# Performance work log

Hardware: AMD Instinct MI355X
Metric: run time of the kernel (lower is better)

The kernel has to match this reference:

```python
import jax, jax.numpy as jnp
import numpy as np

D_MODEL = 768
NUM_HEADS = 12
HEAD_DIM = D_MODEL // NUM_HEADS
LN_EPS = 1e-5
MASK_NEG = -1000000.0


def setup_inputs() -> dict:
    key = jax.random.key(0)
    ks = jax.random.split(key, 10)
    B, L, S = 2, 2048, 2048
    s = 1.0 / np.sqrt(D_MODEL)
    return {
        "q": jax.random.normal(ks[0], (B, L, D_MODEL), jnp.float32),
        "k": jax.random.normal(ks[1], (B, S, D_MODEL), jnp.float32),
        "v": jax.random.normal(ks[2], (B, S, D_MODEL), jnp.float32),
        "attention_mask": jnp.ones((B, S), jnp.int32),
        "Wq": jax.random.normal(ks[3], (D_MODEL, D_MODEL), jnp.float32) * s,
        "Wk": jax.random.normal(ks[4], (D_MODEL, D_MODEL), jnp.float32) * s,
        "Wv": jax.random.normal(ks[5], (D_MODEL, D_MODEL), jnp.float32) * s,
        "W": jax.random.normal(ks[6], (D_MODEL, D_MODEL), jnp.float32) * s,
        "b": jnp.zeros((D_MODEL,), jnp.float32),
        "gamma": jnp.ones((D_MODEL,), jnp.float32),
        "beta": jnp.zeros((D_MODEL,), jnp.float32),
    }


def reference(q, k, v, attention_mask, Wq, Wk, Wv, W, b, gamma, beta):
    B, L, D = q.shape
    S = k.shape[1]
    H, hd = NUM_HEADS, HEAD_DIM
    # projections (torch Linear: x @ W^T), split heads -> (B,H,L,hd)
    Q = (q @ Wq.T).reshape(B, L, H, hd).transpose(0, 2, 1, 3)
    K = (k @ Wk.T).reshape(B, S, H, hd).transpose(0, 2, 1, 3)
    V = (v @ Wv.T).reshape(B, S, H, hd).transpose(0, 2, 1, 3)
    # scores (B,H,L,S) with additive key-padding mask
    scores = jnp.einsum("bhld,bhsd->bhls", Q, K) / np.sqrt(hd)
    mask_score = (1.0 - attention_mask.astype(q.dtype))[:, None, None, :] * MASK_NEG
    att = jax.nn.softmax(scores + mask_score, axis=-1)  # dropout p=0 (eval)
    # attend, merge heads, output projection (with bias)
    O = jnp.einsum("bhls,bhsd->bhld", att, V).transpose(0, 2, 1, 3).reshape(B, L, D)
    O = O @ W.T + b  # state dropout p=0 (eval)
    # residual + LayerNorm
    x = q + O
    mu = jnp.mean(x, axis=-1, keepdims=True)
    var = jnp.mean(jnp.square(x - mu), axis=-1, keepdims=True)
    return (x - mu) * jax.lax.rsqrt(var + LN_EPS) * gamma + beta
```

## Files before the change

### kernel.cpp

```cpp
#include <hip/hip_runtime.h>
#include <hip/hip_bf16.h>
#include <math.h>


typedef unsigned short u16;
typedef unsigned int   u32;
typedef __bf16 bf16x8 __attribute__((ext_vector_type(8)));
typedef float  f32x4  __attribute__((ext_vector_type(4)));

#define DM   768
#define MR   4096
#define WSZ  589824

#define LOG2E 1.44269504089f
#define SM_C  15.0f
#define K1    (0.125f * LOG2E)

__device__ inline u16 bfbits(float f) {
    union { __bf16 b; u16 u; } x; x.b = (__bf16)f; return x.u;
}

__device__ inline uint4 cvt8(const float* src) {
    const float4* p = reinterpret_cast<const float4*>(src);
    float4 a = p[0], b = p[1];
    union { __bf16 h[8]; uint4 v; } u;
    u.h[0] = (__bf16)a.x; u.h[1] = (__bf16)a.y; u.h[2] = (__bf16)a.z; u.h[3] = (__bf16)a.w;
    u.h[4] = (__bf16)b.x; u.h[5] = (__bf16)b.y; u.h[6] = (__bf16)b.z; u.h[7] = (__bf16)b.w;
    return u.v;
}

__device__ inline uint4 cvt8v(float4 a, float4 b) {
    union { __bf16 h[8]; uint4 v; } u;
    u.h[0] = (__bf16)a.x; u.h[1] = (__bf16)a.y; u.h[2] = (__bf16)a.z; u.h[3] = (__bf16)a.w;
    u.h[4] = (__bf16)b.x; u.h[5] = (__bf16)b.y; u.h[6] = (__bf16)b.z; u.h[7] = (__bf16)b.w;
    return u.v;
}

__global__ __launch_bounds__(256) void wcvt(
    const float* __restrict__ w0, const float* __restrict__ w1,
    const float* __restrict__ w2, const float* __restrict__ w3,
    u16* __restrict__ dst)
{
    const float* src = (blockIdx.y == 0) ? w0 : (blockIdx.y == 1) ? w1
                     : (blockIdx.y == 2) ? w2 : w3;
    size_t idx = ((size_t)blockIdx.x * 256 + threadIdx.x) * 8;
    *reinterpret_cast<uint4*>(&dst[(size_t)blockIdx.y * WSZ + idx]) = cvt8(&src[idx]);
}

__global__ __launch_bounds__(256, 2) void gemm_qkv(
    const float* __restrict__ xq, const float* __restrict__ xk, const float* __restrict__ xv,
    const u16* __restrict__ Wb4,
    u16* __restrict__ oq, u16* __restrict__ ok, u16* __restrict__ ov)
{
    const int mode = blockIdx.z;
    const float* X = (mode == 0) ? xq : (mode == 1) ? xk : xv;
    const u16* Wb  = Wb4 + (size_t)mode * WSZ;
    u16* out       = (mode == 0) ? oq : (mode == 1) ? ok : ov;

    __shared__ __attribute__((aligned(16))) u16 As[2][64][72];
    __shared__ __attribute__((aligned(16))) u16 Bs[2][64][72];

    const int tid  = threadIdx.x;
    const int lane = tid & 63;
    const int w    = tid >> 6;
    const int wm   = (w >> 1) * 32;
    const int wn   = (w & 1) * 32;
    const int quad = lane >> 4;
    const int l16  = lane & 15;
    const int tm   = blockIdx.x * 64;
    const int tn   = blockIdx.y * 64;

    const int row0 = tid >> 3,         col0 = (tid & 7) * 8;
    const int row1 = (tid + 256) >> 3, col1 = ((tid + 256) & 7) * 8;

    const float* a0p = &X[(size_t)(tm + row0) * 768 + col0];
    const float* a1p = &X[(size_t)(tm + row1) * 768 + col1];
    const u16*   b0p = &Wb[(size_t)(tn + row0) * 768 + col0];
    const u16*   b1p = &Wb[(size_t)(tn + row1) * 768 + col1];

    f32x4 acc[2][2] = {};

    {
        *reinterpret_cast<uint4*>(&As[0][row0][col0]) = cvt8(a0p);
        *reinterpret_cast<uint4*>(&As[0][row1][col1]) = cvt8(a1p);
        *reinterpret_cast<uint4*>(&Bs[0][row0][col0]) = *reinterpret_cast<const uint4*>(b0p);
        *reinterpret_cast<uint4*>(&Bs[0][row1][col1]) = *reinterpret_cast<const uint4*>(b1p);
    }

    for (int kt = 0; kt < 12; kt++) {
        const int cur = kt & 1;
        __syncthreads();

        float4 af0a, af0b, af1a, af1b; uint4 bt0, bt1;
        if (kt < 11) {
            const int ko = (kt + 1) * 64;
            af0a = *reinterpret_cast<const float4*>(a0p + ko);
            af0b = *reinterpret_cast<const float4*>(a0p + ko + 4);
            af1a = *reinterpret_cast<const float4*>(a1p + ko);
            af1b = *reinterpret_cast<const float4*>(a1p + ko + 4);
            bt0  = *reinterpret_cast<const uint4*>(b0p + ko);
            bt1  = *reinterpret_cast<const uint4*>(b1p + ko);
        }

        #pragma unroll
        for (int kk = 0; kk < 2; kk++) {
            bf16x8 a0 = *reinterpret_cast<const bf16x8*>(&As[cur][wm + l16     ][kk*32 + quad*8]);
            bf16x8 a1 = *reinterpret_cast<const bf16x8*>(&As[cur][wm + 16 + l16][kk*32 + quad*8]);
            bf16x8 b0 = *reinterpret_cast<const bf16x8*>(&Bs[cur][wn + l16     ][kk*32 + quad*8]);
            bf16x8 b1 = *reinterpret_cast<const bf16x8*>(&Bs[cur][wn + 16 + l16][kk*32 + quad*8]);
            acc[0][0] = __builtin_amdgcn_mfma_f32_16x16x32_bf16(a0, b0, acc[0][0], 0, 0, 0);
            acc[0][1] = __builtin_amdgcn_mfma_f32_16x16x32_bf16(a0, b1, acc[0][1], 0, 0, 0);
            acc[1][0] = __builtin_amdgcn_mfma_f32_16x16x32_bf16(a1, b0, acc[1][0], 0, 0, 0);
            acc[1][1] = __builtin_amdgcn_mfma_f32_16x16x32_bf16(a1, b1, acc[1][1], 0, 0, 0);
        }

        if (kt < 11) {
            const int nxt = cur ^ 1;
            *reinterpret_cast<uint4*>(&As[nxt][row0][col0]) = cvt8v(af0a, af0b);
            *reinterpret_cast<uint4*>(&As[nxt][row1][col1]) = cvt8v(af1a, af1b);
            *reinterpret_cast<uint4*>(&Bs[nxt][row0][col0]) = bt0;
            *reinterpret_cast<uint4*>(&Bs[nxt][row1][col1]) = bt1;
        }
    }

    #pragma unroll
    for (int i = 0; i < 2; i++)
        #pragma unroll
        for (int j = 0; j < 2; j++)
            #pragma unroll
            for (int r = 0; r < 4; r++) {
                int gm = tm + wm + i * 16 + quad * 4 + r;
                int gn = tn + wn + j * 16 + l16;
                int b = gm >> 11, l = gm & 2047;
                int h = gn >> 6,  d = gn & 63;
                u16 bv = bfbits(acc[i][j][r]);
                if (mode == 2)
                    out[((size_t)(b * 12 + h) * 64 + d) * 2048 + l] = bv;
                else
                    out[((size_t)(b * 12 + h) * 2048 + l) * 64 + d] = bv;
            }
}

__global__ __launch_bounds__(256, 2) void gemm_out(
    const u16* __restrict__ Oa, const u16* __restrict__ Wb,
    const float* __restrict__ bias, const float* __restrict__ resid,
    float* __restrict__ Xb)
{
    __shared__ __attribute__((aligned(16))) u16 As[2][64][72];
    __shared__ __attribute__((aligned(16))) u16 Bs[2][64][72];

    const int tid  = threadIdx.x;
    const int lane = tid & 63;
    const int w    = tid >> 6;
    const int wm   = (w >> 1) * 32;
    const int wn   = (w & 1) * 32;
    const int quad = lane >> 4;
    const int l16  = lane & 15;
    const int tm   = blockIdx.x * 64;
    const int tn   = blockIdx.y * 64;

    const int row0 = tid >> 3,         col0 = (tid & 7) * 8;
    const int row1 = (tid + 256) >> 3, col1 = ((tid + 256) & 7) * 8;

    const u16* a0p = &Oa[(size_t)(tm + row0) * 768 + col0];
    const u16* a1p = &Oa[(size_t)(tm + row1) * 768 + col1];
    const u16* b0p = &Wb[(size_t)(tn + row0) * 768 + col0];
    const u16* b1p = &Wb[(size_t)(tn + row1) * 768 + col1];

    f32x4 acc[2][2] = {};

    {
        *reinterpret_cast<uint4*>(&As[0][row0][col0]) = *reinterpret_cast<const uint4*>(a0p);
        *reinterpret_cast<uint4*>(&As[0][row1][col1]) = *reinterpret_cast<const uint4*>(a1p);
        *reinterpret_cast<uint4*>(&Bs[0][row0][col0]) = *reinterpret_cast<const uint4*>(b0p);
        *reinterpret_cast<uint4*>(&Bs[0][row1][col1]) = *reinterpret_cast<const uint4*>(b1p);
    }

    for (int kt = 0; kt < 12; kt++) {
        const int cur = kt & 1;
        __syncthreads();

        uint4 at0, at1, bt0, bt1;
        if (kt < 11) {
            const int ko = (kt + 1) * 64;
            at0 = *reinterpret_cast<const uint4*>(a0p + ko);
            at1 = *reinterpret_cast<const uint4*>(a1p + ko);
            bt0 = *reinterpret_cast<const uint4*>(b0p + ko);
            bt1 = *reinterpret_cast<const uint4*>(b1p + ko);
        }

        #pragma unroll
        for (int kk = 0; kk < 2; kk++) {
            bf16x8 a0 = *reinterpret_cast<const bf16x8*>(&As[cur][wm + l16     ][kk*32 + quad*8]);
            bf16x8 a1 = *reinterpret_cast<const bf16x8*>(&As[cur][wm + 16 + l16][kk*32 + quad*8]);
            bf16x8 b0 = *reinterpret_cast<const bf16x8*>(&Bs[cur][wn + l16     ][kk*32 + quad*8]);
            bf16x8 b1 = *reinterpret_cast<const bf16x8*>(&Bs[cur][wn + 16 + l16][kk*32 + quad*8]);
            acc[0][0] = __builtin_amdgcn_mfma_f32_16x16x32_bf16(a0, b0, acc[0][0], 0, 0, 0);
            acc[0][1] = __builtin_amdgcn_mfma_f32_16x16x32_bf16(a0, b1, acc[0][1], 0, 0, 0);
            acc[1][0] = __builtin_amdgcn_mfma_f32_16x16x32_bf16(a1, b0, acc[1][0], 0, 0, 0);
            acc[1][1] = __builtin_amdgcn_mfma_f32_16x16x32_bf16(a1, b1, acc[1][1], 0, 0, 0);
        }

        if (kt < 11) {
            const int nxt = cur ^ 1;
            *reinterpret_cast<uint4*>(&As[nxt][row0][col0]) = at0;
            *reinterpret_cast<uint4*>(&As[nxt][row1][col1]) = at1;
            *reinterpret_cast<uint4*>(&Bs[nxt][row0][col0]) = bt0;
            *reinterpret_cast<uint4*>(&Bs[nxt][row1][col1]) = bt1;
        }
    }

    #pragma unroll
    for (int i = 0; i < 2; i++)
        #pragma unroll
        for (int j = 0; j < 2; j++)
            #pragma unroll
            for (int r = 0; r < 4; r++) {
                int gm = tm + wm + i * 16 + quad * 4 + r;
                int gn = tn + wn + j * 16 + l16;
                Xb[(size_t)gm * 768 + gn] = acc[i][j][r] + bias[gn] + resid[(size_t)gm * 768 + gn];
            }
}

__global__ __launch_bounds__(256, 3) void attn(
    const u16* __restrict__ Qp, const u16* __restrict__ Kp, const u16* __restrict__ Vt,
    const int* __restrict__ amask, u16* __restrict__ Oatt)
{
    __shared__ __attribute__((aligned(16))) unsigned char smem[4 * 64 * 40 * 2 + 2048 * 4];
    u16 (*Ps)[64][40] = reinterpret_cast<u16(*)[64][40]>(smem);
    float* maskC = reinterpret_cast<float*>(smem + 20480);
    float (*Obuf)[72] = reinterpret_cast<float(*)[72]>(smem);

    const int tid  = threadIdx.x;
    const int lane = tid & 63;
    const int w    = tid >> 6;
    const int quad = lane >> 4;
    const int l16  = lane & 15;
    const int qt = blockIdx.x;
    const int h  = blockIdx.y;
    const int b  = blockIdx.z;

    #pragma unroll
    for (int i = 0; i < 8; i++) {
        int s = tid + i * 256;
        maskC[s] = amask[b * 2048 + s] ? (-SM_C * LOG2E) : -2.0e6f;
    }
    __syncthreads();

    const u16* Qbase = Qp + ((size_t)(b * 12 + h) * 2048 + qt * 64) * 64;
    const u16* Kb2   = Kp + (size_t)(b * 12 + h) * 2048 * 64 + (size_t)w * 32 * 64;
    const u16* Vb2   = Vt + (size_t)(b * 12 + h) * 64 * 2048 + (size_t)w * 32;

    bf16x8 qfrag[4][2];
    #pragma unroll
    for (int qb = 0; qb < 4; qb++)
        #pragma unroll
        for (int kk = 0; kk < 2; kk++)
            qfrag[qb][kk] = *reinterpret_cast<const bf16x8*>(
                &Qbase[(qb * 16 + l16) * 64 + kk * 32 + quad * 8]);

    bf16x8 onesf = {};
    if (l16 == 0) {
        #pragma unroll
        for (int i = 0; i < 8; i++) onesf[i] = (__bf16)1.0f;
    }

    f32x4 oacc[4][4] = {};
    f32x4 sacc[4]    = {};

    for (int st = 0; st < 16; st++) {
        bf16x8 kf[2][2], vf[4];
        #pragma unroll
        for (int ct = 0; ct < 2; ct++)
            #pragma unroll
            for (int kk = 0; kk < 2; kk++)
                kf[ct][kk] = *reinterpret_cast<const bf16x8*>(
                    &Kb2[(size_t)(st * 128 + ct * 16 + l16) * 64 + kk * 32 + quad * 8]);
        #pragma unroll
        for (int cd = 0; cd < 4; cd++)
            vf[cd] = *reinterpret_cast<const bf16x8*>(
                &Vb2[(size_t)(cd * 16 + l16) * 2048 + st * 128 + quad * 8]);

        #pragma unroll
        for (int qb = 0; qb < 4; qb++)
            #pragma unroll
            for (int ct = 0; ct < 2; ct++) {
                f32x4 s = {};
                s = __builtin_amdgcn_mfma_f32_16x16x32_bf16(kf[ct][0], qfrag[qb][0], s, 0, 0, 0);
                s = __builtin_amdgcn_mfma_f32_16x16x32_bf16(kf[ct][1], qfrag[qb][1], s, 0, 0, 0);
                f32x4 cc = *reinterpret_cast<const f32x4*>(
                    &maskC[st * 128 + w * 32 + ct * 16 + quad * 4]);
                union { u16 h[4]; uint2 v2; } pk;
                #pragma unroll
                for (int r = 0; r < 4; r++)
                    pk.h[r] = bfbits(__builtin_amdgcn_exp2f(__builtin_fmaf(s[r], K1, cc[r])));
                *reinterpret_cast<uint2*>(&Ps[w][qb * 16 + l16][ct * 16 + quad * 4]) = pk.v2;
            }

        bf16x8 pf[4];
        #pragma unroll
        for (int qb = 0; qb < 4; qb++)
            pf[qb] = *reinterpret_cast<const bf16x8*>(&Ps[w][qb * 16 + l16][quad * 8]);
        #pragma unroll
        for (int qb = 0; qb < 4; qb++)
            sacc[qb] = __builtin_amdgcn_mfma_f32_16x16x32_bf16(pf[qb], onesf, sacc[qb], 0, 0, 0);
        #pragma unroll
        for (int qb = 0; qb < 4; qb++)
            #pragma unroll
            for (int cd = 0; cd < 4; cd++)
                oacc[qb][cd] = __builtin_amdgcn_mfma_f32_16x16x32_bf16(pf[qb], vf[cd], oacc[qb][cd], 0, 0, 0);
    }

    __syncthreads();
    for (int wv = 0; wv < 4; wv++) {
        if (w == wv) {
            #pragma unroll
            for (int qb = 0; qb < 4; qb++) {
                #pragma unroll
                for (int cd = 0; cd < 4; cd++)
                    #pragma unroll
                    for (int r = 0; r < 4; r++) {
                        float* cell = &Obuf[qb * 16 + quad * 4 + r][cd * 16 + l16];
                        if (wv == 0) *cell = oacc[qb][cd][r];
                        else         *cell += oacc[qb][cd][r];
                    }
                if (l16 == 0) {
                    #pragma unroll
                    for (int r = 0; r < 4; r++) {
                        float* cell = &Obuf[qb * 16 + quad * 4 + r][64];
                        if (wv == 0) *cell = sacc[qb][r];
                        else         *cell += sacc[qb][r];
                    }
                }
            }
        }
        __syncthreads();
    }

    #pragma unroll
    for (int g = 0; g < 4; g++) {
        int unit = tid + g * 256;
        int row = unit >> 4;
        int c4  = (unit & 15) * 4;
        float rinv = 1.0f / Obuf[row][64];
        union { u16 h[4]; uint2 v; } o;
        #pragma unroll
        for (int j = 0; j < 4; j++)
            o.h[j] = bfbits(Obuf[row][c4 + j] * rinv);
        *reinterpret_cast<uint2*>(
            &Oatt[(size_t)(b * 2048 + qt * 64 + row) * 768 + h * 64 + c4]) = o.v;
    }
}

__global__ __launch_bounds__(256) void ln_kernel(
    float* __restrict__ X, const float* __restrict__ gamma,
    const float* __restrict__ beta)
{
    const int row = blockIdx.x;
    const int tid = threadIdx.x;
    float* xr = X + (size_t)row * 768;

    float v[3], s = 0.f, s2 = 0.f;
    #pragma unroll
    for (int i = 0; i < 3; i++) {
        v[i] = xr[tid + i * 256];
        s += v[i];
        s2 += v[i] * v[i];
    }
    #pragma unroll
    for (int off = 32; off >= 1; off >>= 1) {
        s  += __shfl_xor(s,  off, 64);
        s2 += __shfl_xor(s2, off, 64);
    }
    __shared__ float rs[4], rs2[4];
    int w = tid >> 6, lane = tid & 63;
    if (lane == 0) { rs[w] = s; rs2[w] = s2; }
    __syncthreads();
    s  = rs[0] + rs[1] + rs[2] + rs[3];
    s2 = rs2[0] + rs2[1] + rs2[2] + rs2[3];
    float mu = s * (1.0f / 768.0f);
    float var = s2 * (1.0f / 768.0f) - mu * mu;
    float rstd = rsqrtf(var + 1e-5f);
    #pragma unroll
    for (int i = 0; i < 3; i++) {
        int c = tid + i * 256;
        xr[c] = (v[i] - mu) * rstd * gamma[c] + beta[c];
    }
}

extern "C" void kernel_launch(void* const* d_in, const int* in_sizes, int n_in,
                              void* d_out, int out_size, void* d_ws, size_t ws_size,
                              hipStream_t stream)
{
    const float* q   = (const float*)d_in[0];
    const float* k   = (const float*)d_in[1];
    const float* v   = (const float*)d_in[2];
    const int*   am  = (const int*)d_in[3];
    const float* Wq  = (const float*)d_in[4];
    const float* Wk  = (const float*)d_in[5];
    const float* Wv  = (const float*)d_in[6];
    const float* W   = (const float*)d_in[7];
    const float* bb  = (const float*)d_in[8];
    const float* gam = (const float*)d_in[9];
    const float* bet = (const float*)d_in[10];

    u16* Wb4 = (u16*)d_ws;
    u16* Qp  = Wb4 + (size_t)4 * WSZ;
    u16* Kp  = Qp + (size_t)MR * DM;
    u16* Vt  = Kp + (size_t)MR * DM;
    u16* Oa  = Vt + (size_t)MR * DM;
    float* Xb = (float*)d_out;

    wcvt<<<dim3(288, 4), 256, 0, stream>>>(Wq, Wk, Wv, W, Wb4);
    gemm_qkv<<<dim3(64, 12, 3), 256, 0, stream>>>(q, k, v, Wb4, Qp, Kp, Vt);
    attn<<<dim3(32, 12, 2), 256, 0, stream>>>(Qp, Kp, Vt, am, Oa);
    gemm_out<<<dim3(64, 12), 256, 0, stream>>>(Oa, Wb4 + (size_t)3 * WSZ, bb, q, Xb);
    ln_kernel<<<4096, 256, 0, stream>>>(Xb, gam, bet);
}
```

Baseline: 218.1 us.

## Add MFMA setprio hints, shrink Obuf padding, use wave-per-row vectorized LayerNorm

Wraps the MFMA sequences in the attention loop with s_setprio so waves issuing matrix ops get scheduling priority over waves doing exp and LDS work. Changes the Obuf row stride from 72 to 68 floats to alter LDS bank mapping in the reduction. Rewrites the LayerNorm kernel so each wavefront handles one row with float4 loads and stores. This drops the shared-memory reduction and __syncthreads, and launches a quarter as many blocks.

```diff
diff --git a/kernel.cpp b/kernel.cpp
--- a/kernel.cpp
+++ b/kernel.cpp
@@ -229,7 +229,7 @@
     __shared__ __attribute__((aligned(16))) unsigned char smem[4 * 64 * 40 * 2 + 2048 * 4];
     u16 (*Ps)[64][40] = reinterpret_cast<u16(*)[64][40]>(smem);
     float* maskC = reinterpret_cast<float*>(smem + 20480);
-    float (*Obuf)[72] = reinterpret_cast<float(*)[72]>(smem);
+    float (*Obuf)[68] = reinterpret_cast<float(*)[68]>(smem);
 
     const int tid  = threadIdx.x;
     const int lane = tid & 63;
@@ -286,8 +286,10 @@
             #pragma unroll
             for (int ct = 0; ct < 2; ct++) {
                 f32x4 s = {};
+                __builtin_amdgcn_s_setprio(1);
                 s = __builtin_amdgcn_mfma_f32_16x16x32_bf16(kf[ct][0], qfrag[qb][0], s, 0, 0, 0);
                 s = __builtin_amdgcn_mfma_f32_16x16x32_bf16(kf[ct][1], qfrag[qb][1], s, 0, 0, 0);
+                __builtin_amdgcn_s_setprio(0);
                 f32x4 cc = *reinterpret_cast<const f32x4*>(
                     &maskC[st * 128 + w * 32 + ct * 16 + quad * 4]);
                 union { u16 h[4]; uint2 v2; } pk;
@@ -301,6 +303,7 @@
         #pragma unroll
         for (int qb = 0; qb < 4; qb++)
             pf[qb] = *reinterpret_cast<const bf16x8*>(&Ps[w][qb * 16 + l16][quad * 8]);
+        __builtin_amdgcn_s_setprio(1);
         #pragma unroll
         for (int qb = 0; qb < 4; qb++)
             sacc[qb] = __builtin_amdgcn_mfma_f32_16x16x32_bf16(pf[qb], onesf, sacc[qb], 0, 0, 0);
@@ -309,6 +312,7 @@
             #pragma unroll
             for (int cd = 0; cd < 4; cd++)
                 oacc[qb][cd] = __builtin_amdgcn_mfma_f32_16x16x32_bf16(pf[qb], vf[cd], oacc[qb][cd], 0, 0, 0);
+        __builtin_amdgcn_s_setprio(0);
     }
 
     __syncthreads();
@@ -356,35 +360,39 @@
     float* __restrict__ X, const float* __restrict__ gamma,
     const float* __restrict__ beta)
 {
-    const int row = blockIdx.x;
-    const int tid = threadIdx.x;
+    const int tid  = threadIdx.x;
+    const int w    = tid >> 6;
+    const int lane = tid & 63;
+    const int row  = blockIdx.x * 4 + w;
     float* xr = X + (size_t)row * 768;
 
-    float v[3], s = 0.f, s2 = 0.f;
+    float4 v[3];
+    float s = 0.f, s2 = 0.f;
     #pragma unroll
     for (int i = 0; i < 3; i++) {
-        v[i] = xr[tid + i * 256];
-        s += v[i];
-        s2 += v[i] * v[i];
+        v[i] = *reinterpret_cast<const float4*>(&xr[i * 256 + lane * 4]);
+        s  += v[i].x + v[i].y + v[i].z + v[i].w;
+        s2 += v[i].x * v[i].x + v[i].y * v[i].y + v[i].z * v[i].z + v[i].w * v[i].w;
     }
     #pragma unroll
     for (int off = 32; off >= 1; off >>= 1) {
         s  += __shfl_xor(s,  off, 64);
         s2 += __shfl_xor(s2, off, 64);
     }
-    __shared__ float rs[4], rs2[4];
-    int w = tid >> 6, lane = tid & 63;
-    if (lane == 0) { rs[w] = s; rs2[w] = s2; }
-    __syncthreads();
-    s  = rs[0] + rs[1] + rs[2] + rs[3];
-    s2 = rs2[0] + rs2[1] + rs2[2] + rs2[3];
-    float mu = s * (1.0f / 768.0f);
+    float mu  = s * (1.0f / 768.0f);
     float var = s2 * (1.0f / 768.0f) - mu * mu;
     float rstd = rsqrtf(var + 1e-5f);
     #pragma unroll
     for (int i = 0; i < 3; i++) {
-        int c = tid + i * 256;
-        xr[c] = (v[i] - mu) * rstd * gamma[c] + beta[c];
+        int c = i * 256 + lane * 4;
+        float4 g  = *reinterpret_cast<const float4*>(&gamma[c]);
+        float4 bt = *reinterpret_cast<const float4*>(&beta[c]);
+        float4 o;
+        o.x = (v[i].x - mu) * rstd * g.x + bt.x;
+        o.y = (v[i].y - mu) * rstd * g.y + bt.y;
+        o.z = (v[i].z - mu) * rstd * g.z + bt.z;
+        o.w = (v[i].w - mu) * rstd * g.w + bt.w;
+        *reinterpret_cast<float4*>(&xr[c]) = o;
     }
 }
 
@@ -415,5 +423,5 @@
     gemm_qkv<<<dim3(64, 12, 3), 256, 0, stream>>>(q, k, v, Wb4, Qp, Kp, Vt);
     attn<<<dim3(32, 12, 2), 256, 0, stream>>>(Qp, Kp, Vt, am, Oa);
     gemm_out<<<dim3(64, 12), 256, 0, stream>>>(Oa, Wb4 + (size_t)3 * WSZ, bb, q, Xb);
-    ln_kernel<<<4096, 256, 0, stream>>>(Xb, gam, bet);
-}
+    ln_kernel<<<1024, 256, 0, stream>>>(Xb, gam, bet);
+}
```

After: 218.1 us. No clear change (-0.0%).
